# Performance work log

Measured on AMD Instinct MI355X. Metric: run time of the kernel, lower is better.

Reference implementation:

```python
import jax, jax.numpy as jnp
import numpy as np

N = 100000
E = 1600000
IN_DIM = 128
HID_DIM = 32
OUT_DIM = 8


def setup_inputs() -> dict:
    key = jax.random.key(0)
    k_x, k_e, k_w1, k_b1, k_w2, k_b2 = jax.random.split(key, 6)
    x = jax.random.normal(k_x, (N, IN_DIM), dtype=jnp.float32)
    edge_index = jax.random.randint(k_e, (2, E), 0, N, dtype=jnp.int64)
    # GCNConv parameters (glorot-ish scale)
    W1 = jax.random.normal(k_w1, (IN_DIM, HID_DIM), dtype=jnp.float32) / np.sqrt(IN_DIM)
    b1 = jnp.zeros((HID_DIM,), dtype=jnp.float32)
    W2 = jax.random.normal(k_w2, (HID_DIM, OUT_DIM), dtype=jnp.float32) / np.sqrt(HID_DIM)
    b2 = jnp.zeros((OUT_DIM,), dtype=jnp.float32)
    return {"x": x, "edge_index": edge_index, "W1": W1, "b1": b1, "W2": W2, "b2": b2}


def _gcn_conv(x, src, dst, norm, W, b, n_nodes):
    # PyG GCNConv: out = D^{-1/2} (A + I) D^{-1/2} X W + b
    h = x @ W                              # [N, F_out] -- transform before aggregation
    msg = h[src] * norm[:, None]           # gather + per-edge normalization, [E+N, F_out]
    out = jax.ops.segment_sum(msg, dst, num_segments=n_nodes)  # scatter-add
    return out + b


def reference(x, edge_index, W1, b1, W2, b2):
    n = x.shape[0]
    loop = jnp.arange(n, dtype=edge_index.dtype)
    src = jnp.concatenate([edge_index[0], loop])   # add self-loops
    dst = jnp.concatenate([edge_index[1], loop])
    # symmetric normalization: deg computed on destination (PyG convention)
    deg = jax.ops.segment_sum(jnp.ones_like(dst, dtype=jnp.float32), dst, num_segments=n)
    deg_inv_sqrt = jax.lax.rsqrt(deg)              # deg >= 1 due to self-loops
    norm = deg_inv_sqrt[src] * deg_inv_sqrt[dst]   # [E+N]
    h = jax.nn.relu(_gcn_conv(x, src, dst, norm, W1, b1, n))
    out = _gcn_conv(h, src, dst, norm, W2, b2, n)
    return out
```

## Files before the change

kernel.cpp:

```cpp
#include <hip/hip_runtime.h>

#define IN_DIM 128
#define HID 32
#define OUTD 8
#define CAP 64

#define NODE_BITS 7
#define NODES_PER_BUK 128
#define MAXNB 1024
#define BUK_CAP 3072
#define BIN_CHUNK 4096
#define BIN_THREADS 512

#define MM1_ROWS 256
#define MM1_KC 32
#define MM1_XS 36

__device__ __forceinline__ float bf2f(unsigned short b) {
    union { unsigned u; float f; } v; v.u = ((unsigned)b) << 16; return v.f;
}
__device__ __forceinline__ unsigned short f2bf(float f) {
    union { float f; unsigned u; } v; v.f = f;
    unsigned r = v.u + 0x7FFF + ((v.u >> 16) & 1);
    return (unsigned short)(r >> 16);
}

__global__ __launch_bounds__(256) void k_zero(int* __restrict__ p, int n) {
    int i = blockIdx.x * 256 + threadIdx.x;
    if (i < n) p[i] = 0;
}

__global__ __launch_bounds__(BIN_THREADS) void k_bin(const int* __restrict__ src,
                                                     const int* __restrict__ dst, int E, int NB,
                                                     int* __restrict__ fillpad,
                                                     int* __restrict__ binned) {
    __shared__ int hist[MAXNB];
    __shared__ int lofs[MAXNB];
    __shared__ int cur[MAXNB];
    __shared__ int bbase[MAXNB];
    __shared__ int stage[BIN_CHUNK];
    __shared__ unsigned short stagebkt[BIN_CHUNK];
    __shared__ int ss[BIN_THREADS];

    int t = threadIdx.x;
    int base = blockIdx.x * BIN_CHUNK;
    int nE = E - base;
    if (nE > BIN_CHUNK) nE = BIN_CHUNK;

    for (int b = t; b < MAXNB; b += BIN_THREADS) hist[b] = 0;
    __syncthreads();

    int dreg[BIN_CHUNK / BIN_THREADS], sreg[BIN_CHUNK / BIN_THREADS];
#pragma unroll
    for (int k = 0; k < BIN_CHUNK / BIN_THREADS; k++) {
        int i = base + t + k * BIN_THREADS;
        dreg[k] = -1;
        if (i < E) {
            dreg[k] = dst[i];
            sreg[k] = src[i];
            atomicAdd(&hist[dreg[k] >> NODE_BITS], 1);
        }
    }
    __syncthreads();

    {
        int v0 = hist[t * 2], v1 = hist[t * 2 + 1];
        int s = v0 + v1;
        ss[t] = s;
        __syncthreads();
        for (int d = 1; d < BIN_THREADS; d <<= 1) {
            int add = (t >= d) ? ss[t - d] : 0;
            __syncthreads();
            ss[t] += add;
            __syncthreads();
        }
        int excl = ss[t] - s;
        lofs[t * 2] = excl; cur[t * 2] = excl;
        excl += v0;
        lofs[t * 2 + 1] = excl; cur[t * 2 + 1] = excl;
    }
    __syncthreads();

    for (int b = t; b < NB; b += BIN_THREADS) {
        int hcnt = hist[b];
        bbase[b] = (hcnt > 0) ? atomicAdd(&fillpad[b * 16], hcnt) : 0;
    }
    __syncthreads();

#pragma unroll
    for (int k = 0; k < BIN_CHUNK / BIN_THREADS; k++) {
        if (dreg[k] >= 0) {
            int b = dreg[k] >> NODE_BITS;
            int slot = atomicAdd(&cur[b], 1);
            stage[slot] = sreg[k] | ((dreg[k] & (NODES_PER_BUK - 1)) << 17);
            stagebkt[slot] = (unsigned short)b;
        }
    }
    __syncthreads();

    for (int p = t; p < nE; p += BIN_THREADS) {
        int b = stagebkt[p];
        int g = bbase[b] + (p - lofs[b]);
        if (g < BUK_CAP) binned[(size_t)b * BUK_CAP + g] = stage[p];
    }
}

__global__ __launch_bounds__(256) void k_bucket2csr(const int* __restrict__ binned,
                                                    const int* __restrict__ fillpad,
                                                    int* __restrict__ csr,
                                                    int* __restrict__ cnt,
                                                    float* __restrict__ dinv, int N) {
    __shared__ int lists[NODES_PER_BUK * CAP];
    __shared__ int lcnt[NODES_PER_BUK];
    __shared__ int smax[4];
    int t = threadIdx.x;
    int b = blockIdx.x;
    int d0 = b * NODES_PER_BUK;
    int nloc = N - d0;
    if (nloc > NODES_PER_BUK) nloc = NODES_PER_BUK;

    if (t < NODES_PER_BUK) lcnt[t] = 0;
    __syncthreads();

    int count = fillpad[b * 16];
    if (count > BUK_CAP) count = BUK_CAP;
    for (int i = t; i < count; i += 256) {
        int v = binned[(size_t)b * BUK_CAP + i];
        int node = (v >> 17) & (NODES_PER_BUK - 1);
        int s = atomicAdd(&lcnt[node], 1);
        if (s < CAP) lists[node * CAP + s] = v & 0x1FFFF;
    }
    __syncthreads();

    int k = (t < nloc) ? lcnt[t] : 0;
    int m = k;
    m = max(m, __shfl_down(m, 32));
    m = max(m, __shfl_down(m, 16));
    m = max(m, __shfl_down(m, 8));
    m = max(m, __shfl_down(m, 4));
    m = max(m, __shfl_down(m, 2));
    m = max(m, __shfl_down(m, 1));
    if ((t & 63) == 0) smax[t >> 6] = m;
    __syncthreads();
    m = min(max(max(smax[0], smax[1]), max(smax[2], smax[3])), CAP);
    int lg = 4;
    if (m > 32) lg = 6;
    else if (m > 16) lg = 5;
    int mxr = 1 << lg;

    if (nloc > 0) {
        int total = nloc << lg;
        size_t gbase = (size_t)d0 * CAP;
        for (int idx = t; idx < total; idx += 256) {
            int n = idx >> lg, s = idx & (mxr - 1);
            csr[gbase + (size_t)n * CAP + s] = lists[n * CAP + s];
        }
        if (t < nloc) {
            cnt[d0 + t] = lcnt[t];
            dinv[d0 + t] = rsqrtf((float)lcnt[t] + 1.0f);
        }
    }
}

__global__ __launch_bounds__(256) void k_count(const int* __restrict__ dst, int E,
                                               int* __restrict__ cnt) {
    int i = blockIdx.x * 256 + threadIdx.x;
    if (i < E) atomicAdd(&cnt[dst[i]], 1);
}

__global__ __launch_bounds__(256) void k_scan_partial(const int* __restrict__ cnt, int N,
                                                      int* __restrict__ bsum) {
    __shared__ int ss[256];
    int t = threadIdx.x;
    int base = blockIdx.x * 1024 + t * 4;
    int s = 0;
#pragma unroll
    for (int k = 0; k < 4; k++) {
        int idx = base + k;
        if (idx < N) s += cnt[idx];
    }
    ss[t] = s;
    __syncthreads();
    for (int d = 128; d > 0; d >>= 1) {
        if (t < d) ss[t] += ss[t + d];
        __syncthreads();
    }
    if (t == 0) bsum[blockIdx.x] = ss[0];
}

__global__ void k_scan_bsums(int* bsum, int nb) {
    if (threadIdx.x == 0 && blockIdx.x == 0) {
        int acc = 0;
        for (int i = 0; i < nb; i++) {
            int v = bsum[i];
            bsum[i] = acc;
            acc += v;
        }
    }
}

__global__ __launch_bounds__(256) void k_scan_final(const int* __restrict__ cnt, int N,
                                                    const int* __restrict__ bsum,
                                                    int* __restrict__ off) {
    __shared__ int ss[256];
    int t = threadIdx.x;
    int base = blockIdx.x * 1024 + t * 4;
    int v[4];
    int s = 0;
#pragma unroll
    for (int k = 0; k < 4; k++) {
        int idx = base + k;
        v[k] = (idx < N) ? cnt[idx] : 0;
        s += v[k];
    }
    ss[t] = s;
    __syncthreads();
    for (int d = 1; d < 256; d <<= 1) {
        int add = (t >= d) ? ss[t - d] : 0;
        __syncthreads();
        ss[t] += add;
        __syncthreads();
    }
    int excl = ss[t] - s + bsum[blockIdx.x];
#pragma unroll
    for (int k = 0; k < 4; k++) {
        int idx = base + k;
        if (idx < N) off[idx] = excl;
        excl += v[k];
        if (idx == N - 1) off[N] = excl;
    }
}

__global__ __launch_bounds__(256) void k_fill_exact(const int* __restrict__ src,
                                                    const int* __restrict__ dst, int E,
                                                    const int* __restrict__ off,
                                                    int* __restrict__ fill, int* __restrict__ csr) {
    int i = blockIdx.x * 256 + threadIdx.x;
    if (i < E) {
        int d = dst[i];
        int p = off[d] + atomicAdd(&fill[d], 1);
        csr[p] = src[i];
    }
}

__global__ __launch_bounds__(256) void k_dinv(const int* __restrict__ cnt, int N,
                                              float* __restrict__ dinv) {
    int i = blockIdx.x * 256 + threadIdx.x;
    if (i < N) dinv[i] = rsqrtf((float)cnt[i] + 1.0f);
}

__global__ __launch_bounds__(512) void k_mm1(const float* __restrict__ x,
                                             const float* __restrict__ W1,
                                             const float* __restrict__ dinv,
                                             unsigned short* __restrict__ g0, int N) {
    __shared__ float Xs[MM1_ROWS][MM1_XS];
    __shared__ float Ws[IN_DIM][HID];
    int t = threadIdx.x;
    int row0 = blockIdx.x * MM1_ROWS;

    {
        const float4* Wv = (const float4*)W1;
        float4* Wsv = (float4*)&Ws[0][0];
#pragma unroll
        for (int i = 0; i < 2; i++) Wsv[t + i * 512] = Wv[t + i * 512];
    }

    int rg = t >> 3, cg = t & 7;
    int r0 = row0 + rg * 4;
    float acc[4][4];
#pragma unroll
    for (int i = 0; i < 4; i++)
#pragma unroll
        for (int j = 0; j < 4; j++) acc[i][j] = 0.0f;

    for (int kc = 0; kc < IN_DIM; kc += MM1_KC) {
        __syncthreads();
#pragma unroll
        for (int p = 0; p < 4; p++) {
            int idx = t + p * 512;
            int r = idx >> 3, q = idx & 7;
            int gr = row0 + r;
            float4 v = make_float4(0.0f, 0.0f, 0.0f, 0.0f);
            if (gr < N) v = *(const float4*)&x[(size_t)gr * IN_DIM + kc + q * 4];
            *(float4*)&Xs[r][q * 4] = v;
        }
        __syncthreads();

#pragma unroll
        for (int k = 0; k < MM1_KC; k += 4) {
            float4 xa[4], wb[4];
#pragma unroll
            for (int i = 0; i < 4; i++) xa[i] = *(const float4*)&Xs[rg * 4 + i][k];
#pragma unroll
            for (int kk = 0; kk < 4; kk++) wb[kk] = *(const float4*)&Ws[kc + k + kk][cg * 4];
#pragma unroll
            for (int i = 0; i < 4; i++) {
                const float* xi = (const float*)&xa[i];
#pragma unroll
                for (int kk = 0; kk < 4; kk++) {
                    float xv = xi[kk];
                    acc[i][0] = fmaf(xv, wb[kk].x, acc[i][0]);
                    acc[i][1] = fmaf(xv, wb[kk].y, acc[i][1]);
                    acc[i][2] = fmaf(xv, wb[kk].z, acc[i][2]);
                    acc[i][3] = fmaf(xv, wb[kk].w, acc[i][3]);
                }
            }
        }
    }

#pragma unroll
    for (int i = 0; i < 4; i++) {
        int r = r0 + i;
        if (r < N) {
            float dv = dinv[r];
            ushort4 o;
            o.x = f2bf(acc[i][0] * dv);
            o.y = f2bf(acc[i][1] * dv);
            o.z = f2bf(acc[i][2] * dv);
            o.w = f2bf(acc[i][3] * dv);
            *(ushort4*)&g0[(size_t)r * HID + cg * 4] = o;
        }
    }
}

template<bool BUCKET>
__global__ __launch_bounds__(256) void k_agg1(const unsigned short* __restrict__ g0,
                                              const int* __restrict__ off,
                                              const int* __restrict__ csr,
                                              const int* __restrict__ cnt,
                                              const float* __restrict__ dinv,
                                              const float* __restrict__ b1,
                                              float* __restrict__ h, int N) {
    int t = threadIdx.x;
    int grp = t >> 4;
    int l = t & 15;
    int d = blockIdx.x * 16 + grp;
    if (d >= N) return;
    long base;
    int deg;
    if (BUCKET) { base = (long)d * CAP; deg = min(cnt[d], CAP); }
    else        { int b = off[d]; base = b; deg = off[d + 1] - b; }
    const unsigned* g0p = (const unsigned*)g0;
    unsigned u = g0p[(size_t)d * (HID / 2) + l];
    float sx = bf2f((unsigned short)(u & 0xffff));
    float sy = bf2f((unsigned short)(u >> 16));
    int p = 0;
    for (; p + 8 <= deg; p += 8) {
        int s0 = csr[base + p + 0], s1 = csr[base + p + 1];
        int s2 = csr[base + p + 2], s3 = csr[base + p + 3];
        int s4 = csr[base + p + 4], s5 = csr[base + p + 5];
        int s6 = csr[base + p + 6], s7 = csr[base + p + 7];
        unsigned u0 = g0p[(size_t)s0 * (HID / 2) + l], u1 = g0p[(size_t)s1 * (HID / 2) + l];
        unsigned u2 = g0p[(size_t)s2 * (HID / 2) + l], u3 = g0p[(size_t)s3 * (HID / 2) + l];
        unsigned u4 = g0p[(size_t)s4 * (HID / 2) + l], u5 = g0p[(size_t)s5 * (HID / 2) + l];
        unsigned u6 = g0p[(size_t)s6 * (HID / 2) + l], u7 = g0p[(size_t)s7 * (HID / 2) + l];
        sx += ((bf2f((unsigned short)(u0 & 0xffff)) + bf2f((unsigned short)(u1 & 0xffff))) +
               (bf2f((unsigned short)(u2 & 0xffff)) + bf2f((unsigned short)(u3 & 0xffff)))) +
              ((bf2f((unsigned short)(u4 & 0xffff)) + bf2f((unsigned short)(u5 & 0xffff))) +
               (bf2f((unsigned short)(u6 & 0xffff)) + bf2f((unsigned short)(u7 & 0xffff))));
        sy += ((bf2f((unsigned short)(u0 >> 16)) + bf2f((unsigned short)(u1 >> 16))) +
               (bf2f((unsigned short)(u2 >> 16)) + bf2f((unsigned short)(u3 >> 16)))) +
              ((bf2f((unsigned short)(u4 >> 16)) + bf2f((unsigned short)(u5 >> 16))) +
               (bf2f((unsigned short)(u6 >> 16)) + bf2f((unsigned short)(u7 >> 16))));
    }
    for (; p < deg; p++) {
        int s = csr[base + p];
        unsigned us = g0p[(size_t)s * (HID / 2) + l];
        sx += bf2f((unsigned short)(us & 0xffff));
        sy += bf2f((unsigned short)(us >> 16));
    }
    float dv = dinv[d];
    float2 o;
    o.x = fmaxf(fmaf(dv, sx, b1[2 * l]), 0.0f);
    o.y = fmaxf(fmaf(dv, sy, b1[2 * l + 1]), 0.0f);
    *(float2*)&h[(size_t)d * HID + 2 * l] = o;
}

__global__ __launch_bounds__(256) void k_mm2(const float* __restrict__ h,
                                             const float* __restrict__ W2,
                                             const float* __restrict__ dinv,
                                             float* __restrict__ g1, int N) {
    __shared__ float Wl[HID * OUTD];
    __shared__ float Hl[32 * 33];
    int t = threadIdx.x;
    if (t < HID * OUTD) Wl[t] = W2[t];
    int row0 = blockIdx.x * 32;
    for (int i = t; i < 32 * HID; i += 256) {
        int r = row0 + i / HID;
        Hl[(i / HID) * 33 + (i % HID)] = (r < N) ? h[(size_t)r * HID + (i % HID)] : 0.0f;
    }
    __syncthreads();
    int lr = t >> 3;
    int j = t & 7;
    int r = row0 + lr;
    float acc = 0.0f;
#pragma unroll
    for (int k = 0; k < HID; k++) acc = fmaf(Hl[lr * 33 + k], Wl[k * OUTD + j], acc);
    if (r < N) g1[(size_t)r * OUTD + j] = dinv[r] * acc;
}

template<bool BUCKET>
__global__ __launch_bounds__(256) void k_agg2(const float* __restrict__ g1,
                                              const int* __restrict__ off,
                                              const int* __restrict__ csr,
                                              const int* __restrict__ cnt,
                                              const float* __restrict__ dinv,
                                              const float* __restrict__ b2,
                                              float* __restrict__ out, int N) {
    int t = threadIdx.x;
    int grp = t >> 3;
    int j = t & 7;
    int d = blockIdx.x * 32 + grp;
    if (d >= N) return;
    long base;
    int deg;
    if (BUCKET) { base = (long)d * CAP; deg = min(cnt[d], CAP); }
    else        { int b = off[d]; base = b; deg = off[d + 1] - b; }
    float sum = g1[(size_t)d * OUTD + j];
    int p = 0;
    for (; p + 8 <= deg; p += 8) {
        int s0 = csr[base + p + 0], s1 = csr[base + p + 1];
        int s2 = csr[base + p + 2], s3 = csr[base + p + 3];
        int s4 = csr[base + p + 4], s5 = csr[base + p + 5];
        int s6 = csr[base + p + 6], s7 = csr[base + p + 7];
        float a0 = g1[(size_t)s0 * OUTD + j], a1 = g1[(size_t)s1 * OUTD + j];
        float a2 = g1[(size_t)s2 * OUTD + j], a3 = g1[(size_t)s3 * OUTD + j];
        float a4 = g1[(size_t)s4 * OUTD + j], a5 = g1[(size_t)s5 * OUTD + j];
        float a6 = g1[(size_t)s6 * OUTD + j], a7 = g1[(size_t)s7 * OUTD + j];
        sum += ((a0 + a1) + (a2 + a3)) + ((a4 + a5) + (a6 + a7));
    }
    for (; p < deg; p++) {
        int s = csr[base + p];
        sum += g1[(size_t)s * OUTD + j];
    }
    out[(size_t)d * OUTD + j] = fmaf(dinv[d], sum, b2[j]);
}

extern "C" void kernel_launch(void* const* d_in, const int* in_sizes, int n_in,
                              void* d_out, int out_size, void* d_ws, size_t ws_size,
                              hipStream_t stream) {
    const float* x  = (const float*)d_in[0];
    const int*   ei = (const int*)d_in[1];
    const float* W1 = (const float*)d_in[2];
    const float* b1 = (const float*)d_in[3];
    const float* W2 = (const float*)d_in[4];
    const float* b2 = (const float*)d_in[5];
    float* out = (float*)d_out;
    (void)n_in; (void)out_size;

    int N = in_sizes[0] / IN_DIM;
    int E = in_sizes[1] / 2;
    const int* src = ei;
    const int* dst = ei + E;
    int NB = (N + NODES_PER_BUK - 1) >> NODE_BITS;

    char* ws = (char*)d_ws;
    size_t o = 0;
    auto give = [&](size_t bytes) -> char* {
        char* p = ws + o;
        o = (o + bytes + 255) & ~(size_t)255;
        return p;
    };

    size_t need_bucket = 0;
    {
        size_t t = 0;
        auto sim = [&](size_t b) { t = (t + b + 255) & ~(size_t)255; };
        sim((size_t)N * 4);
        sim((size_t)N * 4);
        sim((size_t)NB * 16 * 4);
        sim((size_t)N * CAP * 4);
        sim((size_t)N * HID * 4);
        sim((size_t)N * HID * 4);
        sim((size_t)N * OUTD * 4);
        need_bucket = t;
    }

    int gN = (N + 255) / 256;
    int gE = (E + 255) / 256;
    int gMM1 = (N + MM1_ROWS - 1) / MM1_ROWS;
    bool radix_ok = (NB <= MAXNB) &&
                    ((size_t)NB * BUK_CAP * 4 <= (size_t)N * HID * 4) &&
                    (ws_size >= need_bucket);

    if (radix_ok) {
        int*   cnt     = (int*)give((size_t)N * 4);
        float* dinv    = (float*)give((size_t)N * 4);
        int*   fillpad = (int*)give((size_t)NB * 16 * 4);
        int*   csr     = (int*)give((size_t)N * CAP * 4);
        float* g0      = (float*)give((size_t)N * HID * 4);
        float* h       = (float*)give((size_t)N * HID * 4);
        float* g1      = (float*)give((size_t)N * OUTD * 4);
        int*   binned  = (int*)g0;

        int nzero = NB * 16;
        k_zero<<<(nzero + 255) / 256, 256, 0, stream>>>(fillpad, nzero);
        k_bin<<<(E + BIN_CHUNK - 1) / BIN_CHUNK, BIN_THREADS, 0, stream>>>(src, dst, E, NB, fillpad, binned);
        k_bucket2csr<<<NB, 256, 0, stream>>>(binned, fillpad, csr, cnt, dinv, N);
        k_mm1<<<gMM1, 512, 0, stream>>>(x, W1, dinv, (unsigned short*)g0, N);
        k_agg1<true><<<(N + 15) / 16, 256, 0, stream>>>((const unsigned short*)g0, nullptr, csr, cnt, dinv, b1, h, N);
        k_mm2<<<(N + 31) / 32, 256, 0, stream>>>(h, W2, dinv, g1, N);
        k_agg2<true><<<(N + 31) / 32, 256, 0, stream>>>(g1, nullptr, csr, cnt, dinv, b2, out, N);
    } else {
        int*   cnt  = (int*)give((size_t)2 * N * 4);
        int*   fill = cnt + N;
        int*   off  = (int*)give((size_t)(N + 1) * 4);
        int*   bsum = (int*)give(1024 * 4);
        float* dinv = (float*)give((size_t)N * 4);
        int*   csr  = (int*)give((size_t)E * 4);
        float* g0   = (float*)give((size_t)N * HID * 4);
        float* h    = (float*)give((size_t)N * HID * 4);
        float* g1   = (float*)give((size_t)N * OUTD * 4);

        k_zero<<<(2 * N + 255) / 256, 256, 0, stream>>>(cnt, 2 * N);
        int nb = (N + 1023) / 1024;
        k_count<<<gE, 256, 0, stream>>>(dst, E, cnt);
        k_scan_partial<<<nb, 256, 0, stream>>>(cnt, N, bsum);
        k_scan_bsums<<<1, 1, 0, stream>>>(bsum, nb);
        k_scan_final<<<nb, 256, 0, stream>>>(cnt, N, bsum, off);
        k_fill_exact<<<gE, 256, 0, stream>>>(src, dst, E, off, fill, csr);
        k_dinv<<<gN, 256, 0, stream>>>(cnt, N, dinv);
        k_mm1<<<gMM1, 512, 0, stream>>>(x, W1, dinv, (unsigned short*)g0, N);
        k_agg1<false><<<(N + 15) / 16, 256, 0, stream>>>((const unsigned short*)g0, off, csr, cnt, dinv, b1, h, N);
        k_mm2<<<(N + 31) / 32, 256, 0, stream>>>(h, W2, dinv, g1, N);
        k_agg2<false><<<(N + 31) / 32, 256, 0, stream>>>(g1, off, csr, cnt, dinv, b2, out, N);
    }
}
```

Measured before the change: 118.1 us.

## Fuse layer-1 aggregation with second matmul, dropping intermediate h buffer

The first-layer aggregation kernel now also applies bias+ReLU and multiplies by W2 in registers, reducing across 8 lanes with xor shuffles, and writes g1 directly. The separate k_mm2 kernel and the N×32 float h buffer are removed. Each thread now handles 4 features with 8-byte gathers instead of 2 features with 4-byte gathers, so more nodes fit per block. The cost is extra shuffle and ALU work per node and higher register use in the gather kernel.

After: 113.0 us (median of 2 runs). -4.3%, faster.

```diff
diff --git a/kernel.cpp b/kernel.cpp
--- a/kernel.cpp
+++ b/kernel.cpp
@@ -324,79 +324,93 @@
 }
 
 template<bool BUCKET>
-__global__ __launch_bounds__(256) void k_agg1(const unsigned short* __restrict__ g0,
-                                              const int* __restrict__ off,
-                                              const int* __restrict__ csr,
-                                              const int* __restrict__ cnt,
-                                              const float* __restrict__ dinv,
-                                              const float* __restrict__ b1,
-                                              float* __restrict__ h, int N) {
-    int t = threadIdx.x;
-    int grp = t >> 4;
-    int l = t & 15;
-    int d = blockIdx.x * 16 + grp;
+__global__ __launch_bounds__(256) void k_agg1f(const unsigned short* __restrict__ g0,
+                                               const int* __restrict__ off,
+                                               const int* __restrict__ csr,
+                                               const int* __restrict__ cnt,
+                                               const float* __restrict__ dinv,
+                                               const float* __restrict__ b1,
+                                               const float* __restrict__ W2,
+                                               float* __restrict__ g1, int N) {
+    int t = threadIdx.x;
+    int grp = t >> 3;
+    int l = t & 7;
+    int d = blockIdx.x * 32 + grp;
     if (d >= N) return;
     long base;
     int deg;
     if (BUCKET) { base = (long)d * CAP; deg = min(cnt[d], CAP); }
     else        { int b = off[d]; base = b; deg = off[d + 1] - b; }
-    const unsigned* g0p = (const unsigned*)g0;
-    unsigned u = g0p[(size_t)d * (HID / 2) + l];
-    float sx = bf2f((unsigned short)(u & 0xffff));
-    float sy = bf2f((unsigned short)(u >> 16));
+    const uint2* g0p = (const uint2*)g0;
+    uint2 u = g0p[(size_t)d * (HID / 4) + l];
+    float s0 = bf2f((unsigned short)(u.x & 0xffff));
+    float s1 = bf2f((unsigned short)(u.x >> 16));
+    float s2 = bf2f((unsigned short)(u.y & 0xffff));
+    float s3 = bf2f((unsigned short)(u.y >> 16));
     int p = 0;
     for (; p + 8 <= deg; p += 8) {
-        int s0 = csr[base + p + 0], s1 = csr[base + p + 1];
-        int s2 = csr[base + p + 2], s3 = csr[base + p + 3];
-        int s4 = csr[base + p + 4], s5 = csr[base + p + 5];
-        int s6 = csr[base + p + 6], s7 = csr[base + p + 7];
-        unsigned u0 = g0p[(size_t)s0 * (HID / 2) + l], u1 = g0p[(size_t)s1 * (HID / 2) + l];
-        unsigned u2 = g0p[(size_t)s2 * (HID / 2) + l], u3 = g0p[(size_t)s3 * (HID / 2) + l];
-        unsigned u4 = g0p[(size_t)s4 * (HID / 2) + l], u5 = g0p[(size_t)s5 * (HID / 2) + l];
-        unsigned u6 = g0p[(size_t)s6 * (HID / 2) + l], u7 = g0p[(size_t)s7 * (HID / 2) + l];
-        sx += ((bf2f((unsigned short)(u0 & 0xffff)) + bf2f((unsigned short)(u1 & 0xffff))) +
-               (bf2f((unsigned short)(u2 & 0xffff)) + bf2f((unsigned short)(u3 & 0xffff)))) +
-              ((bf2f((unsigned short)(u4 & 0xffff)) + bf2f((unsigned short)(u5 & 0xffff))) +
-               (bf2f((unsigned short)(u6 & 0xffff)) + bf2f((unsigned short)(u7 & 0xffff))));
-        sy += ((bf2f((unsigned short)(u0 >> 16)) + bf2f((unsigned short)(u1 >> 16))) +
-               (bf2f((unsigned short)(u2 >> 16)) + bf2f((unsigned short)(u3 >> 16)))) +
-              ((bf2f((unsigned short)(u4 >> 16)) + bf2f((unsigned short)(u5 >> 16))) +
-               (bf2f((unsigned short)(u6 >> 16)) + bf2f((unsigned short)(u7 >> 16))));
+        int i0 = csr[base + p + 0], i1 = csr[base + p + 1];
+        int i2 = csr[base + p + 2], i3 = csr[base + p + 3];
+        int i4 = csr[base + p + 4], i5 = csr[base + p + 5];
+        int i6 = csr[base + p + 6], i7 = csr[base + p + 7];
+        uint2 v0 = g0p[(size_t)i0 * (HID / 4) + l], v1 = g0p[(size_t)i1 * (HID / 4) + l];
+        uint2 v2 = g0p[(size_t)i2 * (HID / 4) + l], v3 = g0p[(size_t)i3 * (HID / 4) + l];
+        uint2 v4 = g0p[(size_t)i4 * (HID / 4) + l], v5 = g0p[(size_t)i5 * (HID / 4) + l];
+        uint2 v6 = g0p[(size_t)i6 * (HID / 4) + l], v7 = g0p[(size_t)i7 * (HID / 4) + l];
+        s0 += ((bf2f((unsigned short)(v0.x & 0xffff)) + bf2f((unsigned short)(v1.x & 0xffff))) +
+               (bf2f((unsigned short)(v2.x & 0xffff)) + bf2f((unsigned short)(v3.x & 0xffff)))) +
+              ((bf2f((unsigned short)(v4.x & 0xffff)) + bf2f((unsigned short)(v5.x & 0xffff))) +
+               (bf2f((unsigned short)(v6.x & 0xffff)) + bf2f((unsigned short)(v7.x & 0xffff))));
+        s1 += ((bf2f((unsigned short)(v0.x >> 16)) + bf2f((unsigned short)(v1.x >> 16))) +
+               (bf2f((unsigned short)(v2.x >> 16)) + bf2f((unsigned short)(v3.x >> 16)))) +
+              ((bf2f((unsigned short)(v4.x >> 16)) + bf2f((unsigned short)(v5.x >> 16))) +
+               (bf2f((unsigned short)(v6.x >> 16)) + bf2f((unsigned short)(v7.x >> 16))));
+        s2 += ((bf2f((unsigned short)(v0.y & 0xffff)) + bf2f((unsigned short)(v1.y & 0xffff))) +
+               (bf2f((unsigned short)(v2.y & 0xffff)) + bf2f((unsigned short)(v3.y & 0xffff)))) +
+              ((bf2f((unsigned short)(v4.y & 0xffff)) + bf2f((unsigned short)(v5.y & 0xffff))) +
+               (bf2f((unsigned short)(v6.y & 0xffff)) + bf2f((unsigned short)(v7.y & 0xffff))));
+        s3 += ((bf2f((unsigned short)(v0.y >> 16)) + bf2f((unsigned short)(v1.y >> 16))) +
+               (bf2f((unsigned short)(v2.y >> 16)) + bf2f((unsigned short)(v3.y >> 16)))) +
+              ((bf2f((unsigned short)(v4.y >> 16)) + bf2f((unsigned short)(v5.y >> 16))) +
+               (bf2f((unsigned short)(v6.y >> 16)) + bf2f((unsigned short)(v7.y >> 16))));
     }
     for (; p < deg; p++) {
         int s = csr[base + p];
-        unsigned us = g0p[(size_t)s * (HID / 2) + l];
-        sx += bf2f((unsigned short)(us & 0xffff));
-        sy += bf2f((unsigned short)(us >> 16));
+        uint2 vs = g0p[(size_t)s * (HID / 4) + l];
+        s0 += bf2f((unsigned short)(vs.x & 0xffff));
+        s1 += bf2f((unsigned short)(vs.x >> 16));
+        s2 += bf2f((unsigned short)(vs.y & 0xffff));
+        s3 += bf2f((unsigned short)(vs.y >> 16));
     }
     float dv = dinv[d];
-    float2 o;
-    o.x = fmaxf(fmaf(dv, sx, b1[2 * l]), 0.0f);
-    o.y = fmaxf(fmaf(dv, sy, b1[2 * l + 1]), 0.0f);
-    *(float2*)&h[(size_t)d * HID + 2 * l] = o;
-}
-
-__global__ __launch_bounds__(256) void k_mm2(const float* __restrict__ h,
-                                             const float* __restrict__ W2,
-                                             const float* __restrict__ dinv,
-                                             float* __restrict__ g1, int N) {
-    __shared__ float Wl[HID * OUTD];
-    __shared__ float Hl[32 * 33];
-    int t = threadIdx.x;
-    if (t < HID * OUTD) Wl[t] = W2[t];
-    int row0 = blockIdx.x * 32;
-    for (int i = t; i < 32 * HID; i += 256) {
-        int r = row0 + i / HID;
-        Hl[(i / HID) * 33 + (i % HID)] = (r < N) ? h[(size_t)r * HID + (i % HID)] : 0.0f;
-    }
-    __syncthreads();
-    int lr = t >> 3;
-    int j = t & 7;
-    int r = row0 + lr;
-    float acc = 0.0f;
-#pragma unroll
-    for (int k = 0; k < HID; k++) acc = fmaf(Hl[lr * 33 + k], Wl[k * OUTD + j], acc);
-    if (r < N) g1[(size_t)r * OUTD + j] = dinv[r] * acc;
+    float h0 = fmaxf(fmaf(dv, s0, b1[4 * l + 0]), 0.0f);
+    float h1 = fmaxf(fmaf(dv, s1, b1[4 * l + 1]), 0.0f);
+    float h2 = fmaxf(fmaf(dv, s2, b1[4 * l + 2]), 0.0f);
+    float h3 = fmaxf(fmaf(dv, s3, b1[4 * l + 3]), 0.0f);
+
+    const float4* W2v = (const float4*)W2;
+    float pj[8];
+#pragma unroll
+    for (int j = 0; j < 8; j++) pj[j] = 0.0f;
+#pragma unroll
+    for (int i = 0; i < 4; i++) {
+        float hi = (i == 0) ? h0 : (i == 1) ? h1 : (i == 2) ? h2 : h3;
+        float4 wa = W2v[(4 * l + i) * 2];
+        float4 wb = W2v[(4 * l + i) * 2 + 1];
+        pj[0] = fmaf(hi, wa.x, pj[0]); pj[1] = fmaf(hi, wa.y, pj[1]);
+        pj[2] = fmaf(hi, wa.z, pj[2]); pj[3] = fmaf(hi, wa.w, pj[3]);
+        pj[4] = fmaf(hi, wb.x, pj[4]); pj[5] = fmaf(hi, wb.y, pj[5]);
+        pj[6] = fmaf(hi, wb.z, pj[6]); pj[7] = fmaf(hi, wb.w, pj[7]);
+    }
+#pragma unroll
+    for (int m = 1; m < 8; m <<= 1) {
+#pragma unroll
+        for (int j = 0; j < 8; j++) pj[j] += __shfl_xor(pj[j], m);
+    }
+    float mine = pj[0];
+#pragma unroll
+    for (int j = 1; j < 8; j++) mine = (l == j) ? pj[j] : mine;
+    g1[(size_t)d * OUTD + l] = dv * mine;
 }
 
 template<bool BUCKET>
@@ -471,7 +485,6 @@
         sim((size_t)NB * 16 * 4);
         sim((size_t)N * CAP * 4);
         sim((size_t)N * HID * 4);
-        sim((size_t)N * HID * 4);
         sim((size_t)N * OUTD * 4);
         need_bucket = t;
     }
@@ -489,7 +502,6 @@
         int*   fillpad = (int*)give((size_t)NB * 16 * 4);
         int*   csr     = (int*)give((size_t)N * CAP * 4);
         float* g0      = (float*)give((size_t)N * HID * 4);
-        float* h       = (float*)give((size_t)N * HID * 4);
         float* g1      = (float*)give((size_t)N * OUTD * 4);
         int*   binned  = (int*)g0;
 
@@ -498,8 +510,7 @@
         k_bin<<<(E + BIN_CHUNK - 1) / BIN_CHUNK, BIN_THREADS, 0, stream>>>(src, dst, E, NB, fillpad, binned);
         k_bucket2csr<<<NB, 256, 0, stream>>>(binned, fillpad, csr, cnt, dinv, N);
         k_mm1<<<gMM1, 512, 0, stream>>>(x, W1, dinv, (unsigned short*)g0, N);
-        k_agg1<true><<<(N + 15) / 16, 256, 0, stream>>>((const unsigned short*)g0, nullptr, csr, cnt, dinv, b1, h, N);
-        k_mm2<<<(N + 31) / 32, 256, 0, stream>>>(h, W2, dinv, g1, N);
+        k_agg1f<true><<<(N + 31) / 32, 256, 0, stream>>>((const unsigned short*)g0, nullptr, csr, cnt, dinv, b1, W2, g1, N);
         k_agg2<true><<<(N + 31) / 32, 256, 0, stream>>>(g1, nullptr, csr, cnt, dinv, b2, out, N);
     } else {
         int*   cnt  = (int*)give((size_t)2 * N * 4);
@@ -509,7 +520,6 @@
         float* dinv = (float*)give((size_t)N * 4);
         int*   csr  = (int*)give((size_t)E * 4);
         float* g0   = (float*)give((size_t)N * HID * 4);
-        float* h    = (float*)give((size_t)N * HID * 4);
         float* g1   = (float*)give((size_t)N * OUTD * 4);
 
         k_zero<<<(2 * N + 255) / 256, 256, 0, stream>>>(cnt, 2 * N);
@@ -521,8 +531,7 @@
         k_fill_exact<<<gE, 256, 0, stream>>>(src, dst, E, off, fill, csr);
         k_dinv<<<gN, 256, 0, stream>>>(cnt, N, dinv);
         k_mm1<<<gMM1, 512, 0, stream>>>(x, W1, dinv, (unsigned short*)g0, N);
-        k_agg1<false><<<(N + 15) / 16, 256, 0, stream>>>((const unsigned short*)g0, off, csr, cnt, dinv, b1, h, N);
-        k_mm2<<<(N + 31) / 32, 256, 0, stream>>>(h, W2, dinv, g1, N);
+        k_agg1f<false><<<(N + 31) / 32, 256, 0, stream>>>((const unsigned short*)g0, off, csr, cnt, dinv, b1, W2, g1, N);
         k_agg2<false><<<(N + 31) / 32, 256, 0, stream>>>(g1, off, csr, cnt, dinv, b2, out, N);
     }
 }
```
